# Kernel tuning notes

Hardware: AMD Instinct MI355X
Metric: run time of the kernel (lower is better)

The kernel has to match this reference:

```python
import jax, jax.numpy as jnp
import numpy as np

TOP_K = 2

def setup_inputs() -> dict:
    key = jax.random.key(0)
    ks = jax.random.split(key, 8)
    B, S, D = 2, 2048, 1024
    N_r, N_s = 16, 2
    u = jax.random.normal(ks[0], (B, S, D), dtype=jnp.float32)
    centroids = jax.random.normal(ks[1], (N_r, D), dtype=jnp.float32)
    expert_biases = jnp.zeros((N_r,), dtype=jnp.float32)
    # routed expert Linear params: y = u @ W.T + b, W stored [E, d_out, d_in]
    Wr = jax.random.normal(ks[2], (N_r, D, D), dtype=jnp.float32) * (1.0 / np.sqrt(D))
    br = jax.random.normal(ks[3], (N_r, D), dtype=jnp.float32) * 0.01
    Ws = jax.random.normal(ks[4], (N_s, D, D), dtype=jnp.float32) * (1.0 / np.sqrt(D))
    bs = jax.random.normal(ks[5], (N_s, D), dtype=jnp.float32) * 0.01
    return {"u": u, "centroids": centroids, "expert_biases": expert_biases,
            "Wr": Wr, "br": br, "Ws": Ws, "bs": bs}

def reference(u, centroids, expert_biases, Wr, br, Ws, bs):
    N_r = centroids.shape[0]
    N_s = Ws.shape[0]
    # routing scores over experts
    raw_scores = jnp.einsum('bsd,ed->bse', u, centroids)          # [B,S,E]
    s = jax.nn.softmax(raw_scores + expert_biases, axis=-1)
    # scatter top-k softmax values (un-renormalized, as in the source) into gates
    topk_vals, topk_idx = jax.lax.top_k(s, TOP_K)                  # [B,S,K]
    g_topk = jnp.sum(jax.nn.one_hot(topk_idx, N_r, dtype=s.dtype) * topk_vals[..., None], axis=-2)  # [B,S,E]
    # dense per-expert Linear for all tokens, then gated combine (faithful to source)
    xe = jnp.einsum('bsd,eod->bseo', u, Wr) + br                   # [B,S,E,D]
    routed = jnp.einsum('bse,bseo->bso', g_topk, xe)               # [B,S,D]
    # shared experts: mean of N_s dense Linears
    shared = (jnp.einsum('bsd,eod->bso', u, Ws) + jnp.sum(bs, axis=0)) / N_s
    return u + routed + shared
```

## Files before the change

kernel.cpp:

```cpp
#include <hip/hip_runtime.h>

typedef unsigned short u16x8 __attribute__((ext_vector_type(8)));
typedef short          s16x8 __attribute__((ext_vector_type(8)));
typedef float          f32x4 __attribute__((ext_vector_type(4)));

#define NTOK   4096
#define DMODEL 1024
#define NEXP   16
#define TOPK   2
#define BK     32
#define NK     (DMODEL / BK)
#define MAXT   128

__device__ inline unsigned short f2bf(float f) {
    unsigned int x = __float_as_uint(f);
    x += 0x7fffu + ((x >> 16) & 1u);
    return (unsigned short)(x >> 16);
}
__device__ inline float bf2f(unsigned short h) {
    unsigned int x = ((unsigned int)h) << 16;
    return __uint_as_float(x);
}

__device__ inline void gld16(const void* g, void* l) {
    __builtin_amdgcn_global_load_lds(
        (const __attribute__((address_space(1))) void*)g,
        (__attribute__((address_space(3))) void*)l, 16, 0, 0);
}

#define NWR8  (NEXP * DMODEL * DMODEL / 8)
#define NWS8  (DMODEL * DMODEL / 8)
#define NB8   ((NEXP + 1) * DMODEL / 8)
#define RBLK  (NTOK / 4)
#define CBLK  ((NWR8 + NWS8 + NB8 + 255) / 256)

__global__ void prep_kernel(const float* __restrict__ u,
                            const float* __restrict__ cent,
                            const float* __restrict__ ebias,
                            const float* __restrict__ Wr,
                            const float* __restrict__ br,
                            const float* __restrict__ Ws,
                            const float* __restrict__ bs,
                            unsigned short* __restrict__ ub,
                            unsigned short* __restrict__ w17,
                            float* __restrict__ b17,
                            float* __restrict__ topk_g,
                            int*   __restrict__ topk_i) {
    int bid = blockIdx.x;
    if (bid >= RBLK) {
        int id = (bid - RBLK) * 256 + threadIdx.x;
        if (id < NWR8) {
            size_t base = (size_t)id * 8;
            u16x8 o;
#pragma unroll
            for (int i = 0; i < 8; i++) o[i] = f2bf(Wr[base + i]);
            *(u16x8*)&w17[base] = o;
        } else if (id < NWR8 + NWS8) {
            size_t base = (size_t)(id - NWR8) * 8;
            u16x8 o;
#pragma unroll
            for (int i = 0; i < 8; i++)
                o[i] = f2bf(Ws[base + i] + Ws[(size_t)DMODEL * DMODEL + base + i]);
            *(u16x8*)&w17[(size_t)NEXP * DMODEL * DMODEL + base] = o;
        } else if (id < NWR8 + NWS8 + NB8) {
            int base = (id - NWR8 - NWS8) * 8;
#pragma unroll
            for (int i = 0; i < 8; i++) {
                int idx = base + i;
                b17[idx] = idx < NEXP * DMODEL
                    ? br[idx]
                    : bs[idx - NEXP * DMODEL] + bs[idx - NEXP * DMODEL + DMODEL];
            }
        }
        return;
    }
    int wid  = threadIdx.x >> 6;
    int lane = threadIdx.x & 63;
    int t = bid * 4 + wid;
    const float* urow = u + (size_t)t * DMODEL;

    double acc[NEXP];
#pragma unroll
    for (int e = 0; e < NEXP; e++) acc[e] = 0.0;

    for (int j = 0; j < DMODEL / 64; j++) {
        int d = j * 64 + lane;
        float uf = urow[d];
        ub[(size_t)t * DMODEL + d] = f2bf(uf);
        double uv = (double)uf;
#pragma unroll
        for (int e = 0; e < NEXP; e++)
            acc[e] += uv * (double)cent[e * DMODEL + d];
    }
#pragma unroll
    for (int e = 0; e < NEXP; e++) {
        for (int off = 32; off; off >>= 1)
            acc[e] += __shfl_xor(acc[e], off);
    }
    if (lane == 0) {
        double mx = -1e300;
#pragma unroll
        for (int e = 0; e < NEXP; e++) {
            acc[e] += (double)ebias[e];
            if (acc[e] > mx) mx = acc[e];
        }
        double ex[NEXP], den = 0.0;
#pragma unroll
        for (int e = 0; e < NEXP; e++) { ex[e] = exp(acc[e] - mx); den += ex[e]; }
        int i1 = -1, i2 = -1;
        double v1 = -1.0, v2 = -1.0;
        for (int e = 0; e < NEXP; e++) {
            double v = ex[e];
            if (v > v1)      { v2 = v1; i2 = i1; v1 = v; i1 = e; }
            else if (v > v2) { v2 = v;  i2 = e; }
        }
        topk_g[t * 2 + 0] = (float)(v1 / den);
        topk_g[t * 2 + 1] = (float)(v2 / den);
        topk_i[t * 2 + 0] = i1;
        topk_i[t * 2 + 1] = i2;
    }
}

__global__ void build_all(const float* __restrict__ topk_g,
                          const int*   __restrict__ topk_i,
                          int* __restrict__ cnt,
                          int* __restrict__ tokL,
                          float* __restrict__ gateL,
                          int* __restrict__ idL,
                          int* __restrict__ desc,
                          int* __restrict__ numT) {
    __shared__ int scnt[NEXP];
    int tid = threadIdx.x;
    if (tid < NEXP) scnt[tid] = 0;
    __syncthreads();
    for (int id = tid; id < NTOK * TOPK; id += 1024) {
        int e = topk_i[id];
        int pos = atomicAdd(&scnt[e], 1);
        tokL[e * NTOK + pos]  = id >> 1;
        gateL[e * NTOK + pos] = topk_g[id];
        idL[e * NTOK + pos]   = id;
    }
    __syncthreads();
    if (tid == 0) {
        int s = 0;
        for (int mt = 0; mt < NTOK / 128; mt++) desc[s++] = (NEXP << 16) | mt;
        for (int e = 0; e < NEXP; e++) {
            cnt[e] = scnt[e];
            int nt = (scnt[e] + 127) >> 7;
            for (int m = 0; m < nt; m++) desc[s++] = (e << 16) | m;
        }
        numT[0] = s;
    }
}

__global__ __launch_bounds__(256, 3)
void moe_gemm(const unsigned short* __restrict__ ub,
              const unsigned short* __restrict__ w17,
              const float* __restrict__ b17,
              const int*   __restrict__ cnt,
              const int*   __restrict__ tokL,
              const float* __restrict__ gateL,
              const int*   __restrict__ idL,
              const int*   __restrict__ desc,
              const int*   __restrict__ numT,
              const float* __restrict__ u,
              float* __restrict__ out,
              unsigned short* __restrict__ y) {
    int bid = blockIdx.x;
    int tile = bid >> 3;
    int n0 = (bid & 7) * 128;
    if (tile >= numT[0]) return;
    int d = desc[tile];
    int e = d >> 16;
    int row0 = (d & 0xffff) << 7;
    bool is_shared = (e == NEXP);
    int count = is_shared ? NTOK : cnt[e];

    __shared__ __align__(16) unsigned short As[3][128 * BK];
    __shared__ __align__(16) unsigned short Bs[3][128 * BK];

    int t = threadIdx.x;
    int lane = t & 63, wid = t >> 6;
    int wm = wid >> 1, wn = wid & 1;
    int lr = lane & 15, lk4 = lane >> 4;
    int rchunk = (lk4 ^ ((lr >> 1) & 3)) * 8;

    int srow = lane >> 2;
    int scs  = ((lane & 3) ^ ((lane >> 3) & 3)) * 8;

    const int* tl = tokL + e * NTOK;
    const unsigned short* asrc[2];
    const unsigned short* bsrc[2];
    const unsigned short* bb = w17 + (size_t)e * DMODEL * DMODEL + (size_t)n0 * DMODEL;
#pragma unroll
    for (int p = 0; p < 2; p++) {
        int gi = row0 + wid * 32 + p * 16 + srow;
        int tok = is_shared ? gi : tl[gi < count ? gi : count - 1];
        asrc[p] = ub + (size_t)tok * DMODEL + scs;
        bsrc[p] = bb + (size_t)(wid * 32 + p * 16 + srow) * DMODEL + scs;
    }

#define STAGE(buf, kt) do {                                                     \
    int _k0 = (kt) * BK;                                                        \
    _Pragma("unroll")                                                           \
    for (int p = 0; p < 2; p++) {                                               \
        int r = wid * 32 + p * 16;                                              \
        gld16(asrc[p] + _k0, &As[buf][r * BK]);                                 \
        gld16(bsrc[p] + _k0, &Bs[buf][r * BK]);                                 \
    } } while (0)

    f32x4 acc[4][4];
#pragma unroll
    for (int i = 0; i < 4; i++)
#pragma unroll
        for (int j = 0; j < 4; j++)
#pragma unroll
            for (int v = 0; v < 4; v++) acc[i][j][v] = 0.0f;

    STAGE(0, 0);
    STAGE(1, 1);
    asm volatile("s_waitcnt vmcnt(4)" ::: "memory");
    __builtin_amdgcn_s_barrier();

    int cb = 0;
    for (int kt = 0; kt < NK; kt++) {
        int sb = (cb == 0) ? 2 : cb - 1;
        if (kt + 2 < NK) STAGE(sb, kt + 2);

        __builtin_amdgcn_s_setprio(1);
        s16x8 b[4];
#pragma unroll
        for (int j = 0; j < 4; j++)
            b[j] = *(const s16x8*)&Bs[cb][(wn * 64 + j * 16 + lr) * BK + rchunk];
#pragma unroll
        for (int i = 0; i < 4; i++) {
            s16x8 a = *(const s16x8*)&As[cb][(wm * 64 + i * 16 + lr) * BK + rchunk];
#pragma unroll
            for (int j = 0; j < 4; j++)
                acc[i][j] = __builtin_amdgcn_mfma_f32_16x16x32_bf16(a, b[j], acc[i][j], 0, 0, 0);
        }
        __builtin_amdgcn_s_setprio(0);

        if (kt + 2 < NK) asm volatile("s_waitcnt vmcnt(4)" ::: "memory");
        else             asm volatile("s_waitcnt vmcnt(0)" ::: "memory");
        __builtin_amdgcn_s_barrier();
        cb = (cb == 2) ? 0 : cb + 1;
    }
#undef STAGE

    const float* be = b17 + e * DMODEL;
    if (is_shared) {
#pragma unroll
        for (int i = 0; i < 4; i++) {
#pragma unroll
            for (int v = 0; v < 4; v++) {
                int row = row0 + wm * 64 + i * 16 + lk4 * 4 + v;
#pragma unroll
                for (int j = 0; j < 4; j++) {
                    int col = n0 + wn * 64 + j * 16 + lr;
                    size_t idx = (size_t)row * DMODEL + col;
                    out[idx] = u[idx] + 0.5f * (acc[i][j][v] + be[col]);
                }
            }
        }
    } else {
#pragma unroll
        for (int i = 0; i < 4; i++) {
#pragma unroll
            for (int v = 0; v < 4; v++) {
                int gi = row0 + wm * 64 + i * 16 + lk4 * 4 + v;
                if (gi < count) {
                    int id = idL[e * NTOK + gi];
                    float g = gateL[e * NTOK + gi];
                    unsigned short* yr = y + (size_t)id * DMODEL;
#pragma unroll
                    for (int j = 0; j < 4; j++) {
                        int col = n0 + wn * 64 + j * 16 + lr;
                        yr[col] = f2bf(g * (acc[i][j][v] + be[col]));
                    }
                }
            }
        }
    }
}

__global__ void combine_kernel(const unsigned short* __restrict__ y,
                               float* __restrict__ out) {
    int idx = blockIdx.x * 256 + threadIdx.x;
    int tk = idx >> 7;
    int d8 = (idx & 127) * 8;
    size_t base = (size_t)tk * DMODEL + d8;
    u16x8 a = *(const u16x8*)&y[(size_t)(tk * 2) * DMODEL + d8];
    u16x8 b = *(const u16x8*)&y[(size_t)(tk * 2 + 1) * DMODEL + d8];
    f32x4 o0 = *(const f32x4*)&out[base];
    f32x4 o1 = *(const f32x4*)&out[base + 4];
#pragma unroll
    for (int v = 0; v < 4; v++) {
        o0[v] += bf2f(a[v]) + bf2f(b[v]);
        o1[v] += bf2f(a[v + 4]) + bf2f(b[v + 4]);
    }
    *(f32x4*)&out[base] = o0;
    *(f32x4*)&out[base + 4] = o1;
}

extern "C" void kernel_launch(void* const* d_in, const int* in_sizes, int n_in,
                              void* d_out, int out_size, void* d_ws, size_t ws_size,
                              hipStream_t stream) {
    const float* u    = (const float*)d_in[0];
    const float* cent = (const float*)d_in[1];
    const float* eb   = (const float*)d_in[2];
    const float* Wr   = (const float*)d_in[3];
    const float* br   = (const float*)d_in[4];
    const float* Ws   = (const float*)d_in[5];
    const float* bs   = (const float*)d_in[6];
    float* out = (float*)d_out;

    char* ws = (char*)d_ws;
    size_t off = 0;
    auto take = [&](size_t b) { size_t o = off; off += (b + 255) & ~(size_t)255; return o; };
    float* topk_g = (float*)(ws + take(NTOK * TOPK * 4));
    int*   topk_i = (int*)  (ws + take(NTOK * TOPK * 4));
    int*   cnt    = (int*)  (ws + take(64 * 4));
    int*   tokL   = (int*)  (ws + take((size_t)NEXP * NTOK * 4));
    float* gateL  = (float*)(ws + take((size_t)NEXP * NTOK * 4));
    int*   idL    = (int*)  (ws + take((size_t)NEXP * NTOK * 4));
    int*   desc   = (int*)  (ws + take(MAXT * 4));
    int*   numT   = (int*)  (ws + take(64));
    float* b17    = (float*)(ws + take((size_t)(NEXP + 1) * DMODEL * 4));
    unsigned short* ub  = (unsigned short*)(ws + take((size_t)NTOK * DMODEL * 2));
    unsigned short* w17 = (unsigned short*)(ws + take((size_t)(NEXP + 1) * DMODEL * DMODEL * 2));
    unsigned short* y   = (unsigned short*)(ws + take((size_t)NTOK * TOPK * DMODEL * 2));

    prep_kernel<<<RBLK + CBLK, 256, 0, stream>>>(
        u, cent, eb, Wr, br, Ws, bs, ub, w17, b17, topk_g, topk_i);
    build_all<<<1, 1024, 0, stream>>>(topk_g, topk_i, cnt, tokL, gateL, idL, desc, numT);
    moe_gemm<<<8 * MAXT, 256, 0, stream>>>(
        ub, w17, b17, cnt, tokL, gateL, idL, desc, numT, u, out, y);
    combine_kernel<<<(NTOK * DMODEL / 8) / 256, 256, 0, stream>>>(y, out);
}
```

Measured before the change: 109.1 us.

## Shrink MoE GEMM tiles to 64x128 with 2 waves and double buffering

```diff
diff --git a/kernel.cpp b/kernel.cpp
--- a/kernel.cpp
+++ b/kernel.cpp
@@ -10,7 +10,7 @@
 #define TOPK   2
 #define BK     32
 #define NK     (DMODEL / BK)
-#define MAXT   128
+#define MAXT   256
 
 __device__ inline unsigned short f2bf(float f) {
     unsigned int x = __float_as_uint(f);
@@ -143,17 +143,17 @@
     __syncthreads();
     if (tid == 0) {
         int s = 0;
-        for (int mt = 0; mt < NTOK / 128; mt++) desc[s++] = (NEXP << 16) | mt;
+        for (int mt = 0; mt < NTOK / 64; mt++) desc[s++] = (NEXP << 16) | mt;
         for (int e = 0; e < NEXP; e++) {
             cnt[e] = scnt[e];
-            int nt = (scnt[e] + 127) >> 7;
+            int nt = (scnt[e] + 63) >> 6;
             for (int m = 0; m < nt; m++) desc[s++] = (e << 16) | m;
         }
         numT[0] = s;
     }
 }
 
-__global__ __launch_bounds__(256, 3)
+__global__ __launch_bounds__(128, 3)
 void moe_gemm(const unsigned short* __restrict__ ub,
               const unsigned short* __restrict__ w17,
               const float* __restrict__ b17,
@@ -172,16 +172,15 @@
     if (tile >= numT[0]) return;
     int d = desc[tile];
     int e = d >> 16;
-    int row0 = (d & 0xffff) << 7;
+    int row0 = (d & 0xffff) << 6;
     bool is_shared = (e == NEXP);
     int count = is_shared ? NTOK : cnt[e];
 
-    __shared__ __align__(16) unsigned short As[3][128 * BK];
-    __shared__ __align__(16) unsigned short Bs[3][128 * BK];
+    __shared__ __align__(16) unsigned short As[2][64 * BK];
+    __shared__ __align__(16) unsigned short Bs[2][128 * BK];
 
     int t = threadIdx.x;
     int lane = t & 63, wid = t >> 6;
-    int wm = wid >> 1, wn = wid & 1;
     int lr = lane & 15, lk4 = lane >> 4;
     int rchunk = (lk4 ^ ((lr >> 1) & 3)) * 8;
 
@@ -190,24 +189,28 @@
 
     const int* tl = tokL + e * NTOK;
     const unsigned short* asrc[2];
-    const unsigned short* bsrc[2];
+    const unsigned short* bsrc[4];
     const unsigned short* bb = w17 + (size_t)e * DMODEL * DMODEL + (size_t)n0 * DMODEL;
 #pragma unroll
     for (int p = 0; p < 2; p++) {
         int gi = row0 + wid * 32 + p * 16 + srow;
         int tok = is_shared ? gi : tl[gi < count ? gi : count - 1];
         asrc[p] = ub + (size_t)tok * DMODEL + scs;
-        bsrc[p] = bb + (size_t)(wid * 32 + p * 16 + srow) * DMODEL + scs;
+    }
+#pragma unroll
+    for (int p = 0; p < 4; p++) {
+        bsrc[p] = bb + (size_t)(wid * 64 + p * 16 + srow) * DMODEL + scs;
     }
 
 #define STAGE(buf, kt) do {                                                     \
     int _k0 = (kt) * BK;                                                        \
     _Pragma("unroll")                                                           \
-    for (int p = 0; p < 2; p++) {                                               \
-        int r = wid * 32 + p * 16;                                              \
-        gld16(asrc[p] + _k0, &As[buf][r * BK]);                                 \
-        gld16(bsrc[p] + _k0, &Bs[buf][r * BK]);                                 \
-    } } while (0)
+    for (int p = 0; p < 2; p++)                                                 \
+        gld16(asrc[p] + _k0, &As[buf][(wid * 32 + p * 16) * BK]);               \
+    _Pragma("unroll")                                                           \
+    for (int p = 0; p < 4; p++)                                                 \
+        gld16(bsrc[p] + _k0, &Bs[buf][(wid * 64 + p * 16) * BK]);               \
+} while (0)
 
     f32x4 acc[4][4];
 #pragma unroll
@@ -218,33 +221,33 @@
             for (int v = 0; v < 4; v++) acc[i][j][v] = 0.0f;
 
     STAGE(0, 0);
-    STAGE(1, 1);
-    asm volatile("s_waitcnt vmcnt(4)" ::: "memory");
-    __builtin_amdgcn_s_barrier();
-
-    int cb = 0;
+    int cur = 0;
     for (int kt = 0; kt < NK; kt++) {
-        int sb = (cb == 0) ? 2 : cb - 1;
-        if (kt + 2 < NK) STAGE(sb, kt + 2);
+        if (kt + 1 < NK) {
+            STAGE(cur ^ 1, kt + 1);
+            asm volatile("s_waitcnt vmcnt(6)" ::: "memory");
+        } else {
+            asm volatile("s_waitcnt vmcnt(0)" ::: "memory");
+        }
+        __builtin_amdgcn_s_barrier();
 
         __builtin_amdgcn_s_setprio(1);
         s16x8 b[4];
 #pragma unroll
         for (int j = 0; j < 4; j++)
-            b[j] = *(const s16x8*)&Bs[cb][(wn * 64 + j * 16 + lr) * BK + rchunk];
+            b[j] = *(const s16x8*)&Bs[cur][(wid * 64 + j * 16 + lr) * BK + rchunk];
 #pragma unroll
         for (int i = 0; i < 4; i++) {
-            s16x8 a = *(const s16x8*)&As[cb][(wm * 64 + i * 16 + lr) * BK + rchunk];
+            s16x8 a = *(const s16x8*)&As[cur][(i * 16 + lr) * BK + rchunk];
 #pragma unroll
             for (int j = 0; j < 4; j++)
                 acc[i][j] = __builtin_amdgcn_mfma_f32_16x16x32_bf16(a, b[j], acc[i][j], 0, 0, 0);
         }
         __builtin_amdgcn_s_setprio(0);
 
-        if (kt + 2 < NK) asm volatile("s_waitcnt vmcnt(4)" ::: "memory");
-        else             asm volatile("s_waitcnt vmcnt(0)" ::: "memory");
+        asm volatile("" ::: "memory");
         __builtin_amdgcn_s_barrier();
-        cb = (cb == 2) ? 0 : cb + 1;
+        cur ^= 1;
     }
 #undef STAGE
 
@@ -254,10 +257,10 @@
         for (int i = 0; i < 4; i++) {
 #pragma unroll
             for (int v = 0; v < 4; v++) {
-                int row = row0 + wm * 64 + i * 16 + lk4 * 4 + v;
+                int row = row0 + i * 16 + lk4 * 4 + v;
 #pragma unroll
                 for (int j = 0; j < 4; j++) {
-                    int col = n0 + wn * 64 + j * 16 + lr;
+                    int col = n0 + wid * 64 + j * 16 + lr;
                     size_t idx = (size_t)row * DMODEL + col;
                     out[idx] = u[idx] + 0.5f * (acc[i][j][v] + be[col]);
                 }
@@ -268,14 +271,14 @@
         for (int i = 0; i < 4; i++) {
 #pragma unroll
             for (int v = 0; v < 4; v++) {
-                int gi = row0 + wm * 64 + i * 16 + lk4 * 4 + v;
+                int gi = row0 + i * 16 + lk4 * 4 + v;
                 if (gi < count) {
                     int id = idL[e * NTOK + gi];
                     float g = gateL[e * NTOK + gi];
                     unsigned short* yr = y + (size_t)id * DMODEL;
 #pragma unroll
                     for (int j = 0; j < 4; j++) {
-                        int col = n0 + wn * 64 + j * 16 + lr;
+                        int col = n0 + wid * 64 + j * 16 + lr;
                         yr[col] = f2bf(g * (acc[i][j][v] + be[col]));
                     }
                 }
@@ -334,7 +337,7 @@
     prep_kernel<<<RBLK + CBLK, 256, 0, stream>>>(
         u, cent, eb, Wr, br, Ws, bs, ub, w17, b17, topk_g, topk_i);
     build_all<<<1, 1024, 0, stream>>>(topk_g, topk_i, cnt, tokL, gateL, idL, desc, numT);
-    moe_gemm<<<8 * MAXT, 256, 0, stream>>>(
+    moe_gemm<<<8 * MAXT, 128, 0, stream>>>(
         ub, w17, b17, cnt, tokL, gateL, idL, desc, numT, u, out, y);
     combine_kernel<<<(NTOK * DMODEL / 8) / 256, 256, 0, stream>>>(y, out);
 }
```

Measured after the change: 115.0 us. 5.4% more time.

## Split MoE GEMM along K into two halves and reduce partials in combine

Applied to the files above, without the earlier changes.

```diff
diff --git a/kernel.cpp b/kernel.cpp
--- a/kernel.cpp
+++ b/kernel.cpp
@@ -9,7 +9,9 @@
 #define NEXP   16
 #define TOPK   2
 #define BK     32
-#define NK     (DMODEL / BK)
+#define KSPLIT 2
+#define KHALF  (DMODEL / KSPLIT)
+#define NK2    (KHALF / BK)
 #define MAXT   128
 
 __device__ inline unsigned short f2bf(float f) {
@@ -51,16 +53,24 @@
         int id = (bid - RBLK) * 256 + threadIdx.x;
         if (id < NWR8) {
             size_t base = (size_t)id * 8;
+            f32x4 a = *(const f32x4*)&Wr[base];
+            f32x4 b = *(const f32x4*)&Wr[base + 4];
             u16x8 o;
 #pragma unroll
-            for (int i = 0; i < 8; i++) o[i] = f2bf(Wr[base + i]);
+            for (int i = 0; i < 4; i++) { o[i] = f2bf(a[i]); o[i + 4] = f2bf(b[i]); }
             *(u16x8*)&w17[base] = o;
         } else if (id < NWR8 + NWS8) {
             size_t base = (size_t)(id - NWR8) * 8;
+            f32x4 a0 = *(const f32x4*)&Ws[base];
+            f32x4 b0 = *(const f32x4*)&Ws[base + 4];
+            f32x4 a1 = *(const f32x4*)&Ws[(size_t)DMODEL * DMODEL + base];
+            f32x4 b1 = *(const f32x4*)&Ws[(size_t)DMODEL * DMODEL + base + 4];
             u16x8 o;
 #pragma unroll
-            for (int i = 0; i < 8; i++)
-                o[i] = f2bf(Ws[base + i] + Ws[(size_t)DMODEL * DMODEL + base + i]);
+            for (int i = 0; i < 4; i++) {
+                o[i]     = f2bf(a0[i] + a1[i]);
+                o[i + 4] = f2bf(b0[i] + b1[i]);
+            }
             *(u16x8*)&w17[(size_t)NEXP * DMODEL * DMODEL + base] = o;
         } else if (id < NWR8 + NWS8 + NB8) {
             int base = (id - NWR8 - NWS8) * 8;
@@ -153,7 +163,7 @@
     }
 }
 
-__global__ __launch_bounds__(256, 3)
+__global__ __launch_bounds__(256, 4)
 void moe_gemm(const unsigned short* __restrict__ ub,
               const unsigned short* __restrict__ w17,
               const float* __restrict__ b17,
@@ -165,19 +175,23 @@
               const int*   __restrict__ numT,
               const float* __restrict__ u,
               float* __restrict__ out,
-              unsigned short* __restrict__ y) {
+              unsigned short* __restrict__ y,
+              unsigned short* __restrict__ so1) {
     int bid = blockIdx.x;
-    int tile = bid >> 3;
-    int n0 = (bid & 7) * 128;
+    int n0   = (bid & 7) * 128;
+    int tk   = bid >> 3;
+    int tile = tk >> 1;
+    int ks   = tk & 1;
     if (tile >= numT[0]) return;
     int d = desc[tile];
     int e = d >> 16;
     int row0 = (d & 0xffff) << 7;
     bool is_shared = (e == NEXP);
     int count = is_shared ? NTOK : cnt[e];
-
-    __shared__ __align__(16) unsigned short As[3][128 * BK];
-    __shared__ __align__(16) unsigned short Bs[3][128 * BK];
+    int kbase = ks * KHALF;
+
+    __shared__ __align__(16) unsigned short As[2][128 * BK];
+    __shared__ __align__(16) unsigned short Bs[2][128 * BK];
 
     int t = threadIdx.x;
     int lane = t & 63, wid = t >> 6;
@@ -196,8 +210,8 @@
     for (int p = 0; p < 2; p++) {
         int gi = row0 + wid * 32 + p * 16 + srow;
         int tok = is_shared ? gi : tl[gi < count ? gi : count - 1];
-        asrc[p] = ub + (size_t)tok * DMODEL + scs;
-        bsrc[p] = bb + (size_t)(wid * 32 + p * 16 + srow) * DMODEL + scs;
+        asrc[p] = ub + (size_t)tok * DMODEL + kbase + scs;
+        bsrc[p] = bb + (size_t)(wid * 32 + p * 16 + srow) * DMODEL + kbase + scs;
     }
 
 #define STAGE(buf, kt) do {                                                     \
@@ -218,86 +232,107 @@
             for (int v = 0; v < 4; v++) acc[i][j][v] = 0.0f;
 
     STAGE(0, 0);
-    STAGE(1, 1);
-    asm volatile("s_waitcnt vmcnt(4)" ::: "memory");
-    __builtin_amdgcn_s_barrier();
-
-    int cb = 0;
-    for (int kt = 0; kt < NK; kt++) {
-        int sb = (cb == 0) ? 2 : cb - 1;
-        if (kt + 2 < NK) STAGE(sb, kt + 2);
+    int cur = 0;
+    for (int kt = 0; kt < NK2; kt++) {
+        if (kt + 1 < NK2) {
+            STAGE(cur ^ 1, kt + 1);
+            asm volatile("s_waitcnt vmcnt(4)" ::: "memory");
+        } else {
+            asm volatile("s_waitcnt vmcnt(0)" ::: "memory");
+        }
+        __builtin_amdgcn_s_barrier();
 
         __builtin_amdgcn_s_setprio(1);
         s16x8 b[4];
 #pragma unroll
         for (int j = 0; j < 4; j++)
-            b[j] = *(const s16x8*)&Bs[cb][(wn * 64 + j * 16 + lr) * BK + rchunk];
+            b[j] = *(const s16x8*)&Bs[cur][(wn * 64 + j * 16 + lr) * BK + rchunk];
 #pragma unroll
         for (int i = 0; i < 4; i++) {
-            s16x8 a = *(const s16x8*)&As[cb][(wm * 64 + i * 16 + lr) * BK + rchunk];
+            s16x8 a = *(const s16x8*)&As[cur][(wm * 64 + i * 16 + lr) * BK + rchunk];
 #pragma unroll
             for (int j = 0; j < 4; j++)
                 acc[i][j] = __builtin_amdgcn_mfma_f32_16x16x32_bf16(a, b[j], acc[i][j], 0, 0, 0);
         }
         __builtin_amdgcn_s_setprio(0);
 
-        if (kt + 2 < NK) asm volatile("s_waitcnt vmcnt(4)" ::: "memory");
-        else             asm volatile("s_waitcnt vmcnt(0)" ::: "memory");
+        asm volatile("" ::: "memory");
         __builtin_amdgcn_s_barrier();
-        cb = (cb == 2) ? 0 : cb + 1;
+        cur ^= 1;
     }
 #undef STAGE
 
     const float* be = b17 + e * DMODEL;
     if (is_shared) {
-#pragma unroll
-        for (int i = 0; i < 4; i++) {
-#pragma unroll
-            for (int v = 0; v < 4; v++) {
-                int row = row0 + wm * 64 + i * 16 + lk4 * 4 + v;
-#pragma unroll
-                for (int j = 0; j < 4; j++) {
-                    int col = n0 + wn * 64 + j * 16 + lr;
-                    size_t idx = (size_t)row * DMODEL + col;
-                    out[idx] = u[idx] + 0.5f * (acc[i][j][v] + be[col]);
+        if (ks == 0) {
+#pragma unroll
+            for (int i = 0; i < 4; i++)
+#pragma unroll
+                for (int v = 0; v < 4; v++) {
+                    int row = row0 + wm * 64 + i * 16 + lk4 * 4 + v;
+#pragma unroll
+                    for (int j = 0; j < 4; j++) {
+                        int col = n0 + wn * 64 + j * 16 + lr;
+                        size_t idx = (size_t)row * DMODEL + col;
+                        out[idx] = u[idx] + 0.5f * (acc[i][j][v] + be[col]);
+                    }
                 }
-            }
+        } else {
+#pragma unroll
+            for (int i = 0; i < 4; i++)
+#pragma unroll
+                for (int v = 0; v < 4; v++) {
+                    int row = row0 + wm * 64 + i * 16 + lk4 * 4 + v;
+#pragma unroll
+                    for (int j = 0; j < 4; j++) {
+                        int col = n0 + wn * 64 + j * 16 + lr;
+                        so1[(size_t)row * DMODEL + col] = f2bf(acc[i][j][v]);
+                    }
+                }
         }
     } else {
-#pragma unroll
-        for (int i = 0; i < 4; i++) {
+        unsigned short* yk = y + (size_t)ks * NTOK * TOPK * DMODEL;
+#pragma unroll
+        for (int i = 0; i < 4; i++)
 #pragma unroll
             for (int v = 0; v < 4; v++) {
                 int gi = row0 + wm * 64 + i * 16 + lk4 * 4 + v;
                 if (gi < count) {
                     int id = idL[e * NTOK + gi];
                     float g = gateL[e * NTOK + gi];
-                    unsigned short* yr = y + (size_t)id * DMODEL;
+                    unsigned short* yr = yk + (size_t)id * DMODEL;
 #pragma unroll
                     for (int j = 0; j < 4; j++) {
                         int col = n0 + wn * 64 + j * 16 + lr;
-                        yr[col] = f2bf(g * (acc[i][j][v] + be[col]));
+                        float val = (ks == 0) ? g * (acc[i][j][v] + be[col])
+                                              : g * acc[i][j][v];
+                        yr[col] = f2bf(val);
                     }
                 }
             }
-        }
     }
 }
 
 __global__ void combine_kernel(const unsigned short* __restrict__ y,
+                               const unsigned short* __restrict__ so1,
                                float* __restrict__ out) {
     int idx = blockIdx.x * 256 + threadIdx.x;
     int tk = idx >> 7;
     int d8 = (idx & 127) * 8;
     size_t base = (size_t)tk * DMODEL + d8;
-    u16x8 a = *(const u16x8*)&y[(size_t)(tk * 2) * DMODEL + d8];
-    u16x8 b = *(const u16x8*)&y[(size_t)(tk * 2 + 1) * DMODEL + d8];
+    const unsigned short* y1 = y + (size_t)NTOK * TOPK * DMODEL;
+    u16x8 a0 = *(const u16x8*)&y [(size_t)(tk * 2) * DMODEL + d8];
+    u16x8 a1 = *(const u16x8*)&y1[(size_t)(tk * 2) * DMODEL + d8];
+    u16x8 b0 = *(const u16x8*)&y [(size_t)(tk * 2 + 1) * DMODEL + d8];
+    u16x8 b1 = *(const u16x8*)&y1[(size_t)(tk * 2 + 1) * DMODEL + d8];
+    u16x8 s1 = *(const u16x8*)&so1[base];
     f32x4 o0 = *(const f32x4*)&out[base];
     f32x4 o1 = *(const f32x4*)&out[base + 4];
 #pragma unroll
     for (int v = 0; v < 4; v++) {
-        o0[v] += bf2f(a[v]) + bf2f(b[v]);
-        o1[v] += bf2f(a[v + 4]) + bf2f(b[v + 4]);
+        o0[v] += 0.5f * bf2f(s1[v]) + bf2f(a0[v]) + bf2f(a1[v]) + bf2f(b0[v]) + bf2f(b1[v]);
+        o1[v] += 0.5f * bf2f(s1[v + 4]) + bf2f(a0[v + 4]) + bf2f(a1[v + 4])
+               + bf2f(b0[v + 4]) + bf2f(b1[v + 4]);
     }
     *(f32x4*)&out[base] = o0;
     *(f32x4*)&out[base + 4] = o1;
@@ -329,12 +364,13 @@
     float* b17    = (float*)(ws + take((size_t)(NEXP + 1) * DMODEL * 4));
     unsigned short* ub  = (unsigned short*)(ws + take((size_t)NTOK * DMODEL * 2));
     unsigned short* w17 = (unsigned short*)(ws + take((size_t)(NEXP + 1) * DMODEL * DMODEL * 2));
-    unsigned short* y   = (unsigned short*)(ws + take((size_t)NTOK * TOPK * DMODEL * 2));
+    unsigned short* y   = (unsigned short*)(ws + take((size_t)KSPLIT * NTOK * TOPK * DMODEL * 2));
+    unsigned short* so1 = (unsigned short*)(ws + take((size_t)NTOK * DMODEL * 2));
 
     prep_kernel<<<RBLK + CBLK, 256, 0, stream>>>(
         u, cent, eb, Wr, br, Ws, bs, ub, w17, b17, topk_g, topk_i);
     build_all<<<1, 1024, 0, stream>>>(topk_g, topk_i, cnt, tokL, gateL, idL, desc, numT);
-    moe_gemm<<<8 * MAXT, 256, 0, stream>>>(
-        ub, w17, b17, cnt, tokL, gateL, idL, desc, numT, u, out, y);
-    combine_kernel<<<(NTOK * DMODEL / 8) / 256, 256, 0, stream>>>(y, out);
-}
+    moe_gemm<<<8 * 2 * MAXT, 256, 0, stream>>>(
+        ub, w17, b17, cnt, tokL, gateL, idL, desc, numT, u, out, y, so1);
+    combine_kernel<<<(NTOK * DMODEL / 8) / 256, 256, 0, stream>>>(y, so1, out);
+}
```

New measurement: 117.3 us. 1.07x slower.

## Switch GEMM to double-buffered LDS with higher occupancy, vectorize weight conversion

Applied to the files above, without the earlier changes.

```diff
diff --git a/kernel.cpp b/kernel.cpp
--- a/kernel.cpp
+++ b/kernel.cpp
@@ -51,16 +51,24 @@
         int id = (bid - RBLK) * 256 + threadIdx.x;
         if (id < NWR8) {
             size_t base = (size_t)id * 8;
+            f32x4 a = *(const f32x4*)&Wr[base];
+            f32x4 b = *(const f32x4*)&Wr[base + 4];
             u16x8 o;
 #pragma unroll
-            for (int i = 0; i < 8; i++) o[i] = f2bf(Wr[base + i]);
+            for (int i = 0; i < 4; i++) { o[i] = f2bf(a[i]); o[i + 4] = f2bf(b[i]); }
             *(u16x8*)&w17[base] = o;
         } else if (id < NWR8 + NWS8) {
             size_t base = (size_t)(id - NWR8) * 8;
+            f32x4 a0 = *(const f32x4*)&Ws[base];
+            f32x4 b0 = *(const f32x4*)&Ws[base + 4];
+            f32x4 a1 = *(const f32x4*)&Ws[(size_t)DMODEL * DMODEL + base];
+            f32x4 b1 = *(const f32x4*)&Ws[(size_t)DMODEL * DMODEL + base + 4];
             u16x8 o;
 #pragma unroll
-            for (int i = 0; i < 8; i++)
-                o[i] = f2bf(Ws[base + i] + Ws[(size_t)DMODEL * DMODEL + base + i]);
+            for (int i = 0; i < 4; i++) {
+                o[i]     = f2bf(a0[i] + a1[i]);
+                o[i + 4] = f2bf(b0[i] + b1[i]);
+            }
             *(u16x8*)&w17[(size_t)NEXP * DMODEL * DMODEL + base] = o;
         } else if (id < NWR8 + NWS8 + NB8) {
             int base = (id - NWR8 - NWS8) * 8;
@@ -153,7 +161,7 @@
     }
 }
 
-__global__ __launch_bounds__(256, 3)
+__global__ __launch_bounds__(256, 4)
 void moe_gemm(const unsigned short* __restrict__ ub,
               const unsigned short* __restrict__ w17,
               const float* __restrict__ b17,
@@ -176,8 +184,8 @@
     bool is_shared = (e == NEXP);
     int count = is_shared ? NTOK : cnt[e];
 
-    __shared__ __align__(16) unsigned short As[3][128 * BK];
-    __shared__ __align__(16) unsigned short Bs[3][128 * BK];
+    __shared__ __align__(16) unsigned short As[2][128 * BK];
+    __shared__ __align__(16) unsigned short Bs[2][128 * BK];
 
     int t = threadIdx.x;
     int lane = t & 63, wid = t >> 6;
@@ -218,33 +226,33 @@
             for (int v = 0; v < 4; v++) acc[i][j][v] = 0.0f;
 
     STAGE(0, 0);
-    STAGE(1, 1);
-    asm volatile("s_waitcnt vmcnt(4)" ::: "memory");
-    __builtin_amdgcn_s_barrier();
-
-    int cb = 0;
+    int cur = 0;
     for (int kt = 0; kt < NK; kt++) {
-        int sb = (cb == 0) ? 2 : cb - 1;
-        if (kt + 2 < NK) STAGE(sb, kt + 2);
+        if (kt + 1 < NK) {
+            STAGE(cur ^ 1, kt + 1);
+            asm volatile("s_waitcnt vmcnt(4)" ::: "memory");
+        } else {
+            asm volatile("s_waitcnt vmcnt(0)" ::: "memory");
+        }
+        __builtin_amdgcn_s_barrier();
 
         __builtin_amdgcn_s_setprio(1);
         s16x8 b[4];
 #pragma unroll
         for (int j = 0; j < 4; j++)
-            b[j] = *(const s16x8*)&Bs[cb][(wn * 64 + j * 16 + lr) * BK + rchunk];
+            b[j] = *(const s16x8*)&Bs[cur][(wn * 64 + j * 16 + lr) * BK + rchunk];
 #pragma unroll
         for (int i = 0; i < 4; i++) {
-            s16x8 a = *(const s16x8*)&As[cb][(wm * 64 + i * 16 + lr) * BK + rchunk];
+            s16x8 a = *(const s16x8*)&As[cur][(wm * 64 + i * 16 + lr) * BK + rchunk];
 #pragma unroll
             for (int j = 0; j < 4; j++)
                 acc[i][j] = __builtin_amdgcn_mfma_f32_16x16x32_bf16(a, b[j], acc[i][j], 0, 0, 0);
         }
         __builtin_amdgcn_s_setprio(0);
 
-        if (kt + 2 < NK) asm volatile("s_waitcnt vmcnt(4)" ::: "memory");
-        else             asm volatile("s_waitcnt vmcnt(0)" ::: "memory");
+        asm volatile("" ::: "memory");
         __builtin_amdgcn_s_barrier();
-        cb = (cb == 2) ? 0 : cb + 1;
+        cur ^= 1;
     }
 #undef STAGE
 
```

Measured after the change: 100.0 us. 1.09x faster.
